# Kernel tuning notes

Measured on AMD Instinct MI355X. Metric: run time of the kernel, lower is better.

## Reference

```python
import jax, jax.numpy as jnp
import numpy as np

N_NODES = 100000


def _sage_conv(x, src, dst, w_self, w_neigh, b):
    # DGL SAGEConv('mean'): fc_self(x) + fc_neigh(mean of in-neighbor feats) + bias
    msgs = x[src]                                        # [E, d] gather
    agg = jax.ops.segment_sum(msgs, dst, num_segments=N_NODES)   # [N, d]
    deg = jax.ops.segment_sum(jnp.ones_like(dst, dtype=x.dtype), dst,
                              num_segments=N_NODES)      # [N]
    mean = agg / jnp.maximum(deg, 1.0)[:, None]          # zero-degree -> 0
    return x @ w_self + mean @ w_neigh + b


def setup_inputs() -> dict:
    key = jax.random.key(0)
    ks = jax.random.split(key, 8)
    E, D_IN, D_HID, D_OUT = 1000000, 64, 64, 32
    features = jax.random.normal(ks[0], (N_NODES, D_IN), dtype=jnp.float32)
    src = jax.random.randint(ks[1], (E,), 0, N_NODES, dtype=jnp.int32)
    dst = jax.random.randint(ks[2], (E,), 0, N_NODES, dtype=jnp.int32)
    s = lambda k, i, o: jax.random.normal(k, (i, o), dtype=jnp.float32) / np.sqrt(i)
    return {
        "features": features, "src": src, "dst": dst,
        "w_self1": s(ks[3], D_IN, D_HID), "w_neigh1": s(ks[4], D_IN, D_HID),
        "b1": jnp.zeros((D_HID,), jnp.float32),
        "w_self2": s(ks[5], D_HID, D_OUT), "w_neigh2": s(ks[6], D_HID, D_OUT),
        "b2": jnp.zeros((D_OUT,), jnp.float32),
    }


def reference(features, src, dst, w_self1, w_neigh1, b1, w_self2, w_neigh2, b2):
    h = _sage_conv(features, src, dst, w_self1, w_neigh1, b1)
    h = jax.nn.relu(h)
    # dropout: identity (inference mode)
    h = _sage_conv(h, src, dst, w_self2, w_neigh2, b2)
    return h
```

## Files before the change

### kernel.cpp

```cpp
#include <hip/hip_runtime.h>


#define SPAN        128
#define SPAN_SHIFT  7
#define PART_BLOCK  1024
#define PART_EPT    4
#define NBMAX       1024
#define LDS_S       72

typedef __attribute__((ext_vector_type(8))) short bf16x8;
typedef __attribute__((ext_vector_type(4))) float f32x4;

__device__ __forceinline__ unsigned bf16_rne(float f) {
    unsigned u = __float_as_uint(f);
    return (u + 0x7FFFu + ((u >> 16) & 1u)) >> 16;
}
__device__ __forceinline__ float bf_lo(unsigned u) { return __uint_as_float(u << 16); }
__device__ __forceinline__ float bf_hi(unsigned u) { return __uint_as_float(u & 0xFFFF0000u); }

__global__ __launch_bounds__(PART_BLOCK) void k_partition(
    const int* __restrict__ src, const int* __restrict__ dst,
    int* __restrict__ cursor, unsigned int* __restrict__ pairs,
    int E, int cap,
    const float* __restrict__ feat, unsigned short* __restrict__ xh, long total8,
    const float* __restrict__ ws1, const float* __restrict__ wn1,
    const float* __restrict__ ws2, const float* __restrict__ wn2,
    unsigned short* __restrict__ wt)
{
    const int tid = threadIdx.x;
    for (long i = (long)blockIdx.x * PART_BLOCK + tid; i < total8;
         i += (long)gridDim.x * PART_BLOCK) {
        const float4 a = ((const float4*)feat)[i * 2];
        const float4 b = ((const float4*)feat)[i * 2 + 1];
        uint4 o;
        o.x = bf16_rne(a.x) | (bf16_rne(a.y) << 16);
        o.y = bf16_rne(a.z) | (bf16_rne(a.w) << 16);
        o.z = bf16_rne(b.x) | (bf16_rne(b.y) << 16);
        o.w = bf16_rne(b.z) | (bf16_rne(b.w) << 16);
        ((uint4*)xh)[i] = o;
    }
    if (blockIdx.x < 12) {
        int j = blockIdx.x * PART_BLOCK + tid;
        int mat = j >> 12, rem = j & 4095;
        int c = rem >> 6, k = rem & 63;
        float v;
        if (mat == 0)      v = ws1[k * 64 + c];
        else if (mat == 1) v = wn1[k * 64 + c];
        else               v = (c < 32) ? wn2[k * 32 + c] : ws2[k * 32 + (c - 32)];
        wt[(mat << 12) + (c << 6) + k] = (unsigned short)bf16_rne(v);
    }

    __shared__ int cnt[NBMAX];
    __shared__ int gbase[NBMAX];
    __shared__ int lcur[NBMAX];
    cnt[tid] = 0; lcur[tid] = 0;
    __syncthreads();

    int sv[PART_EPT], bv[PART_EPT];
    const int e0 = blockIdx.x * (PART_BLOCK * PART_EPT) + tid;
    #pragma unroll
    for (int j = 0; j < PART_EPT; ++j) {
        int e = e0 + j * PART_BLOCK;
        bv[j] = -1;
        if (e < E) {
            int s = src[e], d = dst[e];
            bv[j] = d >> SPAN_SHIFT;
            sv[j] = s | ((d & (SPAN - 1)) << 24);
            atomicAdd(&cnt[bv[j]], 1);
        }
    }
    __syncthreads();
    if (cnt[tid] > 0) gbase[tid] = atomicAdd(&cursor[tid], cnt[tid]);
    __syncthreads();
    #pragma unroll
    for (int j = 0; j < PART_EPT; ++j) {
        if (bv[j] >= 0) {
            int r = gbase[bv[j]] + atomicAdd(&lcur[bv[j]], 1);
            if (r < cap) pairs[(size_t)bv[j] * cap + r] = (unsigned int)sv[j];
        }
    }
}

__global__ __launch_bounds__(256) void k_bucket_csr(
    unsigned int* __restrict__ pairs,
    const int* __restrict__ cursor,
    int* __restrict__ starts, int* __restrict__ degs,
    int N, int cap)
{
    __shared__ int cnt[SPAN];
    __shared__ int pref[SPAN];
    __shared__ int lcur[SPAN];
    extern __shared__ unsigned int sorted[];
    const int tid = threadIdx.x;
    const int b = blockIdx.x;
    if (tid < SPAN) { cnt[tid] = 0; lcur[tid] = 0; }
    __syncthreads();

    int m = cursor[b]; if (m > cap) m = cap;
    const size_t pb = (size_t)b * cap;

    for (int i = tid; i < m; i += 256)
        atomicAdd(&cnt[pairs[pb + i] >> 24], 1);
    __syncthreads();

    if (tid < SPAN) pref[tid] = cnt[tid];
    __syncthreads();
    for (int off = 1; off < SPAN; off <<= 1) {
        int v = 0;
        if (tid < SPAN && tid >= off) v = pref[tid - off];
        __syncthreads();
        if (tid < SPAN) pref[tid] += v;
        __syncthreads();
    }

    for (int i = tid; i < m; i += 256) {
        unsigned int p = pairs[pb + i];
        int r = p >> 24;
        int base = (r == 0) ? 0 : pref[r - 1];
        int pos = base + atomicAdd(&lcur[r], 1);
        sorted[pos] = p & 0xFFFFFFu;
    }
    __syncthreads();
    for (int i = tid; i < m; i += 256) pairs[pb + i] = sorted[i];
    if (tid < SPAN) {
        int node = (b << SPAN_SHIFT) + tid;
        if (node < N) {
            int base = (tid == 0) ? 0 : pref[tid - 1];
            starts[node] = (int)pb + base;
            degs[node]   = cnt[tid];
        }
    }
}

__global__ __launch_bounds__(256) void k_gather_fused(
    const unsigned short* __restrict__ xh,
    const unsigned int* __restrict__ esrc,
    const int* __restrict__ starts, const int* __restrict__ degs,
    const unsigned short* __restrict__ wt,
    const float* __restrict__ b1, const float* __restrict__ b2,
    unsigned short* __restrict__ t2,
    float* __restrict__ outp,
    int n)
{
    __shared__ __align__(16) unsigned short sM[32 * LDS_S];
    __shared__ __align__(16) unsigned short sH[32 * LDS_S];
    const int w = threadIdx.x >> 6, lane = threadIdx.x & 63;
    const int quad = lane >> 4, lm = lane & 15;
    const int half = lane >> 5;
    const int q    = (lane >> 3) & 3;
    const int c    = lane & 7;
    const int gm0  = blockIdx.x * 32;
    const int v0   = gm0 + w * 8;

    int e[4], end[4], dg[4];
    #pragma unroll
    for (int j = 0; j < 4; ++j) {
        int v = v0 + j * 2 + half;
        if (v < n) { int b = starts[v]; dg[j] = degs[v]; e[j] = b + q; end[j] = b + dg[j]; }
        else { dg[j] = 0; e[j] = 0; end[j] = 0; }
    }
    float ga[4][8];
    #pragma unroll
    for (int j = 0; j < 4; ++j)
        #pragma unroll
        for (int k = 0; k < 8; ++k) ga[j][k] = 0.f;

    while ((e[0] < end[0]) | (e[1] < end[1]) | (e[2] < end[2]) | (e[3] < end[3])) {
        uint4 u[4]; float m[4];
        #pragma unroll
        for (int j = 0; j < 4; ++j) {
            bool p = e[j] < end[j];
            m[j] = p ? 1.f : 0.f;
            int idx = p ? e[j] : 0;
            int s = (int)(esrc[idx] & 0xFFFFFFu);
            s = s < n ? s : n - 1;
            u[j] = *(const uint4*)&xh[(size_t)s * 64 + c * 8];
        }
        #pragma unroll
        for (int j = 0; j < 4; ++j) {
            ga[j][0] = fmaf(m[j], bf_lo(u[j].x), ga[j][0]);
            ga[j][1] = fmaf(m[j], bf_hi(u[j].x), ga[j][1]);
            ga[j][2] = fmaf(m[j], bf_lo(u[j].y), ga[j][2]);
            ga[j][3] = fmaf(m[j], bf_hi(u[j].y), ga[j][3]);
            ga[j][4] = fmaf(m[j], bf_lo(u[j].z), ga[j][4]);
            ga[j][5] = fmaf(m[j], bf_hi(u[j].z), ga[j][5]);
            ga[j][6] = fmaf(m[j], bf_lo(u[j].w), ga[j][6]);
            ga[j][7] = fmaf(m[j], bf_hi(u[j].w), ga[j][7]);
            e[j] += 4;
        }
    }
    #pragma unroll
    for (int j = 0; j < 4; ++j) {
        #pragma unroll
        for (int d = 8; d <= 16; d <<= 1) {
            #pragma unroll
            for (int k = 0; k < 8; ++k) ga[j][k] += __shfl_xor(ga[j][k], d);
        }
        int v = v0 + j * 2 + half;
        if ((lane & 24) == 0 && v < n) {
            float f = dg[j] ? 1.f / (float)dg[j] : 0.f;
            uint4 o;
            o.x = bf16_rne(ga[j][0] * f) | (bf16_rne(ga[j][1] * f) << 16);
            o.y = bf16_rne(ga[j][2] * f) | (bf16_rne(ga[j][3] * f) << 16);
            o.z = bf16_rne(ga[j][4] * f) | (bf16_rne(ga[j][5] * f) << 16);
            o.w = bf16_rne(ga[j][6] * f) | (bf16_rne(ga[j][7] * f) << 16);
            *(uint4*)&sM[(w * 8 + j * 2 + half) * LDS_S + c * 8] = o;
        }
    }
    __syncthreads();

    f32x4 acc1[2];
    acc1[0] = (f32x4){0.f, 0.f, 0.f, 0.f};
    acc1[1] = (f32x4){0.f, 0.f, 0.f, 0.f};
    #pragma unroll
    for (int mt = 0; mt < 2; ++mt) {
        const int rowG = gm0 + mt * 16 + lm;
        const int rA = rowG < n ? rowG : n - 1;
        #pragma unroll
        for (int kt = 0; kt < 2; ++kt) {
            bf16x8 a  = *(const bf16x8*)&xh[(size_t)rA * 64 + kt * 32 + quad * 8];
            bf16x8 am = *(const bf16x8*)&sM[(mt * 16 + lm) * LDS_S + kt * 32 + quad * 8];
            bf16x8 bs = *(const bf16x8*)&wt[((w * 16 + lm) << 6) + kt * 32 + quad * 8];
            bf16x8 bn = *(const bf16x8*)&wt[(1 << 12) + ((w * 16 + lm) << 6) + kt * 32 + quad * 8];
            acc1[mt] = __builtin_amdgcn_mfma_f32_16x16x32_bf16(a,  bs, acc1[mt], 0, 0, 0);
            acc1[mt] = __builtin_amdgcn_mfma_f32_16x16x32_bf16(am, bn, acc1[mt], 0, 0, 0);
        }
    }
    {
        float bb = b1[w * 16 + lm];
        #pragma unroll
        for (int mt = 0; mt < 2; ++mt) {
            #pragma unroll
            for (int r = 0; r < 4; ++r) {
                float hv = fmaxf(acc1[mt][r] + bb, 0.f);
                sH[(mt * 16 + quad * 4 + r) * LDS_S + w * 16 + lm] =
                    (unsigned short)bf16_rne(hv);
            }
        }
    }
    __syncthreads();

    f32x4 acc2[2];
    acc2[0] = (f32x4){0.f, 0.f, 0.f, 0.f};
    acc2[1] = (f32x4){0.f, 0.f, 0.f, 0.f};
    #pragma unroll
    for (int mt = 0; mt < 2; ++mt) {
        #pragma unroll
        for (int kt = 0; kt < 2; ++kt) {
            bf16x8 a = *(const bf16x8*)&sH[(mt * 16 + lm) * LDS_S + kt * 32 + quad * 8];
            bf16x8 b = *(const bf16x8*)&wt[(2 << 12) + ((w * 16 + lm) << 6) + kt * 32 + quad * 8];
            acc2[mt] = __builtin_amdgcn_mfma_f32_16x16x32_bf16(a, b, acc2[mt], 0, 0, 0);
        }
    }
    #pragma unroll
    for (int mt = 0; mt < 2; ++mt) {
        if (w < 2) {
            #pragma unroll
            for (int r = 0; r < 4; ++r) {
                int gm = gm0 + mt * 16 + quad * 4 + r;
                if (gm < n)
                    t2[(size_t)gm * 32 + w * 16 + lm] = (unsigned short)bf16_rne(acc2[mt][r]);
            }
        } else {
            float bb = b2[(w - 2) * 16 + lm];
            #pragma unroll
            for (int r = 0; r < 4; ++r) {
                int gm = gm0 + mt * 16 + quad * 4 + r;
                if (gm < n)
                    outp[(size_t)gm * 32 + (w - 2) * 16 + lm] = acc2[mt][r] + bb;
            }
        }
    }
}

__global__ __launch_bounds__(256) void k_gather_b32add(
    const unsigned short* __restrict__ t2,
    const unsigned int* __restrict__ esrc,
    const int* __restrict__ starts, const int* __restrict__ degs,
    float* __restrict__ outp, int n)
{
    const int w = threadIdx.x >> 6, lane = threadIdx.x & 63;
    const int half = lane >> 5;
    const int q    = (lane >> 3) & 3;
    const int c    = lane & 7;
    const int v0 = (blockIdx.x * 4 + w) * 8;
    if (v0 >= n) return;

    int e[4], end[4], dg[4];
    #pragma unroll
    for (int j = 0; j < 4; ++j) {
        int v = v0 + j * 2 + half;
        if (v < n) { int b = starts[v]; dg[j] = degs[v]; e[j] = b + q; end[j] = b + dg[j]; }
        else { dg[j] = 0; e[j] = 0; end[j] = 0; }
    }
    float ga[4][4];
    #pragma unroll
    for (int j = 0; j < 4; ++j)
        #pragma unroll
        for (int k = 0; k < 4; ++k) ga[j][k] = 0.f;

    while ((e[0] < end[0]) | (e[1] < end[1]) | (e[2] < end[2]) | (e[3] < end[3])) {
        uint2 u[4]; float m[4];
        #pragma unroll
        for (int j = 0; j < 4; ++j) {
            bool p = e[j] < end[j];
            m[j] = p ? 1.f : 0.f;
            int idx = p ? e[j] : 0;
            int s = (int)(esrc[idx] & 0xFFFFFFu);
            s = s < n ? s : n - 1;
            u[j] = *(const uint2*)&t2[(size_t)s * 32 + c * 4];
        }
        #pragma unroll
        for (int j = 0; j < 4; ++j) {
            ga[j][0] = fmaf(m[j], bf_lo(u[j].x), ga[j][0]);
            ga[j][1] = fmaf(m[j], bf_hi(u[j].x), ga[j][1]);
            ga[j][2] = fmaf(m[j], bf_lo(u[j].y), ga[j][2]);
            ga[j][3] = fmaf(m[j], bf_hi(u[j].y), ga[j][3]);
            e[j] += 4;
        }
    }
    #pragma unroll
    for (int j = 0; j < 4; ++j) {
        #pragma unroll
        for (int d = 8; d <= 16; d <<= 1) {
            #pragma unroll
            for (int k = 0; k < 4; ++k) ga[j][k] += __shfl_xor(ga[j][k], d);
        }
        int v = v0 + j * 2 + half;
        if ((lane & 24) == 0 && v < n && dg[j] > 0) {
            float f = 1.f / (float)dg[j];
            float4 o = *(const float4*)&outp[(size_t)v * 32 + c * 4];
            o.x += ga[j][0] * f; o.y += ga[j][1] * f;
            o.z += ga[j][2] * f; o.w += ga[j][3] * f;
            *(float4*)&outp[(size_t)v * 32 + c * 4] = o;
        }
    }
}

extern "C" void kernel_launch(void* const* d_in, const int* in_sizes, int n_in,
                              void* d_out, int out_size, void* d_ws, size_t ws_size,
                              hipStream_t stream) {
    const float* feat = (const float*)d_in[0];
    const int*   src  = (const int*)d_in[1];
    const int*   dst  = (const int*)d_in[2];
    const float* ws1  = (const float*)d_in[3];
    const float* wn1  = (const float*)d_in[4];
    const float* b1   = (const float*)d_in[5];
    const float* ws2  = (const float*)d_in[6];
    const float* wn2  = (const float*)d_in[7];
    const float* b2   = (const float*)d_in[8];
    float* out = (float*)d_out;

    const int N = in_sizes[0] / 64;
    const int E = in_sizes[1];
    const int nB = (N + SPAN - 1) >> SPAN_SHIFT;

    int cap = ((E + nB - 1) / nB);
    cap = ((cap + cap / 4) + 63) & ~63;
    {
        size_t fixedBytes = NBMAX * 4 + 3 * 4096 * 2 + (size_t)N * 8
                          + (size_t)N * 64 * 2
                          + (size_t)N * 32 * 2
                          + 16384;
        size_t remain = (ws_size > fixedBytes) ? (ws_size - fixedBytes) : 0;
        size_t capMax = remain / ((size_t)nB * 4);
        if ((size_t)cap > capMax) cap = (int)(capMax & ~(size_t)3);
    }

    char* base = (char*)d_ws;
    int* cursor = (int*)base;
    unsigned short* wt = (unsigned short*)(base + NBMAX * 4);
    unsigned int* pairs = (unsigned int*)(base + NBMAX * 4 + 24576);
    size_t sOff = ((size_t)NBMAX * 4 + 24576 + (size_t)nB * cap * 4 + 4096 + 255) & ~(size_t)255;
    int* starts = (int*)(base + sOff);
    int* degs   = starts + N;
    size_t mOff = (sOff + (size_t)N * 8 + 255) & ~(size_t)255;
    unsigned short* xh = (unsigned short*)(base + mOff);
    unsigned short* t2 = xh + (size_t)N * 64;

    hipMemsetAsync(cursor, 0, NBMAX * 4, stream);

    const long total8 = (long)N * 64 / 8;
    const int pblocks = (E + PART_BLOCK * PART_EPT - 1) / (PART_BLOCK * PART_EPT);
    k_partition<<<pblocks, PART_BLOCK, 0, stream>>>(
        src, dst, cursor, pairs, E, cap,
        feat, xh, total8, ws1, wn1, ws2, wn2, wt);
    k_bucket_csr<<<nB, 256, (size_t)cap * 4, stream>>>(pairs, cursor, starts, degs, N, cap);

    const int fblocks = (N + 31) / 32;

    k_gather_fused<<<fblocks, 256, 0, stream>>>(
        xh, pairs, starts, degs, wt, b1, b2, t2, out, N);
    k_gather_b32add<<<fblocks, 256, 0, stream>>>(t2, pairs, starts, degs, out, N);
}
```

Baseline: 181.5 us.

## Fuse per-bucket CSR sort into both gather kernels using LDS-resident edge lists

Removes the separate bucket-CSR kernel and the global starts/degs arrays. Each gather block instead re-sorts its 128-node bucket's edges into shared memory and reads the neighbour indices from LDS. This saves a kernel launch and a global write/read pass over the pairs, but every bucket is now sorted redundantly by 4 blocks in each of two kernels. Dynamic LDS of up to 8KB per block may also reduce occupancy. Capping cap at 2048 risks dropping edges if a bucket overflows.

Measured after the change: 183.8 us. No clear change (+1.3%).

```diff
diff --git a/kernel.cpp b/kernel.cpp
--- a/kernel.cpp
+++ b/kernel.cpp
@@ -81,28 +81,40 @@
     }
 }
 
-__global__ __launch_bounds__(256) void k_bucket_csr(
-    unsigned int* __restrict__ pairs,
+__global__ __launch_bounds__(256) void k_gather_fused(
+    const unsigned short* __restrict__ xh,
+    const unsigned int* __restrict__ pairs,
     const int* __restrict__ cursor,
-    int* __restrict__ starts, int* __restrict__ degs,
-    int N, int cap)
+    const unsigned short* __restrict__ wt,
+    const float* __restrict__ b1, const float* __restrict__ b2,
+    unsigned short* __restrict__ t2,
+    float* __restrict__ outp,
+    int n, int cap)
 {
+    __shared__ __align__(16) unsigned short sM[32 * LDS_S];
+    __shared__ __align__(16) unsigned short sH[32 * LDS_S];
     __shared__ int cnt[SPAN];
     __shared__ int pref[SPAN];
     __shared__ int lcur[SPAN];
     extern __shared__ unsigned int sorted[];
-    const int tid = threadIdx.x;
-    const int b = blockIdx.x;
+    const int tid  = threadIdx.x;
+    const int w    = tid >> 6, lane = tid & 63;
+    const int quad = lane >> 4, lm = lane & 15;
+    const int half = lane >> 5;
+    const int q    = (lane >> 3) & 3;
+    const int c    = lane & 7;
+    const int gm0  = blockIdx.x * 32;
+    const int B    = gm0 >> SPAN_SHIFT;
+    const int dbase = gm0 & (SPAN - 1);
+
     if (tid < SPAN) { cnt[tid] = 0; lcur[tid] = 0; }
-    __syncthreads();
-
-    int m = cursor[b]; if (m > cap) m = cap;
-    const size_t pb = (size_t)b * cap;
-
+    if (tid == 0) sorted[0] = 0;
+    __syncthreads();
+    int m = cursor[B]; if (m > cap) m = cap;
+    const size_t pb = (size_t)B * cap;
     for (int i = tid; i < m; i += 256)
         atomicAdd(&cnt[pairs[pb + i] >> 24], 1);
     __syncthreads();
-
     if (tid < SPAN) pref[tid] = cnt[tid];
     __syncthreads();
     for (int off = 1; off < SPAN; off <<= 1) {
@@ -112,52 +124,25 @@
         if (tid < SPAN) pref[tid] += v;
         __syncthreads();
     }
-
     for (int i = tid; i < m; i += 256) {
         unsigned int p = pairs[pb + i];
         int r = p >> 24;
-        int base = (r == 0) ? 0 : pref[r - 1];
-        int pos = base + atomicAdd(&lcur[r], 1);
-        sorted[pos] = p & 0xFFFFFFu;
-    }
-    __syncthreads();
-    for (int i = tid; i < m; i += 256) pairs[pb + i] = sorted[i];
-    if (tid < SPAN) {
-        int node = (b << SPAN_SHIFT) + tid;
-        if (node < N) {
-            int base = (tid == 0) ? 0 : pref[tid - 1];
-            starts[node] = (int)pb + base;
-            degs[node]   = cnt[tid];
-        }
-    }
-}
-
-__global__ __launch_bounds__(256) void k_gather_fused(
-    const unsigned short* __restrict__ xh,
-    const unsigned int* __restrict__ esrc,
-    const int* __restrict__ starts, const int* __restrict__ degs,
-    const unsigned short* __restrict__ wt,
-    const float* __restrict__ b1, const float* __restrict__ b2,
-    unsigned short* __restrict__ t2,
-    float* __restrict__ outp,
-    int n)
-{
-    __shared__ __align__(16) unsigned short sM[32 * LDS_S];
-    __shared__ __align__(16) unsigned short sH[32 * LDS_S];
-    const int w = threadIdx.x >> 6, lane = threadIdx.x & 63;
-    const int quad = lane >> 4, lm = lane & 15;
-    const int half = lane >> 5;
-    const int q    = (lane >> 3) & 3;
-    const int c    = lane & 7;
-    const int gm0  = blockIdx.x * 32;
-    const int v0   = gm0 + w * 8;
-
+        int base = r ? pref[r - 1] : 0;
+        sorted[base + atomicAdd(&lcur[r], 1)] = p & 0xFFFFFFu;
+    }
+    __syncthreads();
+
+    const int v0 = gm0 + w * 8;
     int e[4], end[4], dg[4];
     #pragma unroll
     for (int j = 0; j < 4; ++j) {
-        int v = v0 + j * 2 + half;
-        if (v < n) { int b = starts[v]; dg[j] = degs[v]; e[j] = b + q; end[j] = b + dg[j]; }
-        else { dg[j] = 0; e[j] = 0; end[j] = 0; }
+        int no = w * 8 + j * 2 + half;
+        int v  = gm0 + no;
+        int dl = dbase + no;
+        if (v < n) {
+            int bb = dl ? pref[dl - 1] : 0;
+            dg[j] = cnt[dl]; e[j] = bb + q; end[j] = bb + dg[j];
+        } else { dg[j] = 0; e[j] = 0; end[j] = 0; }
     }
     float ga[4][8];
     #pragma unroll
@@ -166,26 +151,26 @@
         for (int k = 0; k < 8; ++k) ga[j][k] = 0.f;
 
     while ((e[0] < end[0]) | (e[1] < end[1]) | (e[2] < end[2]) | (e[3] < end[3])) {
-        uint4 u[4]; float m[4];
+        uint4 u[4]; float mm[4];
         #pragma unroll
         for (int j = 0; j < 4; ++j) {
             bool p = e[j] < end[j];
-            m[j] = p ? 1.f : 0.f;
+            mm[j] = p ? 1.f : 0.f;
             int idx = p ? e[j] : 0;
-            int s = (int)(esrc[idx] & 0xFFFFFFu);
+            int s = (int)sorted[idx];
             s = s < n ? s : n - 1;
             u[j] = *(const uint4*)&xh[(size_t)s * 64 + c * 8];
         }
         #pragma unroll
         for (int j = 0; j < 4; ++j) {
-            ga[j][0] = fmaf(m[j], bf_lo(u[j].x), ga[j][0]);
-            ga[j][1] = fmaf(m[j], bf_hi(u[j].x), ga[j][1]);
-            ga[j][2] = fmaf(m[j], bf_lo(u[j].y), ga[j][2]);
-            ga[j][3] = fmaf(m[j], bf_hi(u[j].y), ga[j][3]);
-            ga[j][4] = fmaf(m[j], bf_lo(u[j].z), ga[j][4]);
-            ga[j][5] = fmaf(m[j], bf_hi(u[j].z), ga[j][5]);
-            ga[j][6] = fmaf(m[j], bf_lo(u[j].w), ga[j][6]);
-            ga[j][7] = fmaf(m[j], bf_hi(u[j].w), ga[j][7]);
+            ga[j][0] = fmaf(mm[j], bf_lo(u[j].x), ga[j][0]);
+            ga[j][1] = fmaf(mm[j], bf_hi(u[j].x), ga[j][1]);
+            ga[j][2] = fmaf(mm[j], bf_lo(u[j].y), ga[j][2]);
+            ga[j][3] = fmaf(mm[j], bf_hi(u[j].y), ga[j][3]);
+            ga[j][4] = fmaf(mm[j], bf_lo(u[j].z), ga[j][4]);
+            ga[j][5] = fmaf(mm[j], bf_hi(u[j].z), ga[j][5]);
+            ga[j][6] = fmaf(mm[j], bf_lo(u[j].w), ga[j][6]);
+            ga[j][7] = fmaf(mm[j], bf_hi(u[j].w), ga[j][7]);
             e[j] += 4;
         }
     }
@@ -275,23 +260,59 @@
 
 __global__ __launch_bounds__(256) void k_gather_b32add(
     const unsigned short* __restrict__ t2,
-    const unsigned int* __restrict__ esrc,
-    const int* __restrict__ starts, const int* __restrict__ degs,
-    float* __restrict__ outp, int n)
+    const unsigned int* __restrict__ pairs,
+    const int* __restrict__ cursor,
+    float* __restrict__ outp, int n, int cap)
 {
-    const int w = threadIdx.x >> 6, lane = threadIdx.x & 63;
+    __shared__ int cnt[SPAN];
+    __shared__ int pref[SPAN];
+    __shared__ int lcur[SPAN];
+    extern __shared__ unsigned int sorted[];
+    const int tid  = threadIdx.x;
+    const int w    = tid >> 6, lane = tid & 63;
     const int half = lane >> 5;
     const int q    = (lane >> 3) & 3;
     const int c    = lane & 7;
-    const int v0 = (blockIdx.x * 4 + w) * 8;
-    if (v0 >= n) return;
-
+    const int gm0  = blockIdx.x * 32;
+    const int B    = gm0 >> SPAN_SHIFT;
+    const int dbase = gm0 & (SPAN - 1);
+
+    if (tid < SPAN) { cnt[tid] = 0; lcur[tid] = 0; }
+    if (tid == 0) sorted[0] = 0;
+    __syncthreads();
+    int m = cursor[B]; if (m > cap) m = cap;
+    const size_t pb = (size_t)B * cap;
+    for (int i = tid; i < m; i += 256)
+        atomicAdd(&cnt[pairs[pb + i] >> 24], 1);
+    __syncthreads();
+    if (tid < SPAN) pref[tid] = cnt[tid];
+    __syncthreads();
+    for (int off = 1; off < SPAN; off <<= 1) {
+        int v = 0;
+        if (tid < SPAN && tid >= off) v = pref[tid - off];
+        __syncthreads();
+        if (tid < SPAN) pref[tid] += v;
+        __syncthreads();
+    }
+    for (int i = tid; i < m; i += 256) {
+        unsigned int p = pairs[pb + i];
+        int r = p >> 24;
+        int base = r ? pref[r - 1] : 0;
+        sorted[base + atomicAdd(&lcur[r], 1)] = p & 0xFFFFFFu;
+    }
+    __syncthreads();
+
+    const int v0 = gm0 + w * 8;
     int e[4], end[4], dg[4];
     #pragma unroll
     for (int j = 0; j < 4; ++j) {
-        int v = v0 + j * 2 + half;
-        if (v < n) { int b = starts[v]; dg[j] = degs[v]; e[j] = b + q; end[j] = b + dg[j]; }
-        else { dg[j] = 0; e[j] = 0; end[j] = 0; }
+        int no = w * 8 + j * 2 + half;
+        int v  = gm0 + no;
+        int dl = dbase + no;
+        if (v < n) {
+            int bb = dl ? pref[dl - 1] : 0;
+            dg[j] = cnt[dl]; e[j] = bb + q; end[j] = bb + dg[j];
+        } else { dg[j] = 0; e[j] = 0; end[j] = 0; }
     }
     float ga[4][4];
     #pragma unroll
@@ -300,22 +321,22 @@
         for (int k = 0; k < 4; ++k) ga[j][k] = 0.f;
 
     while ((e[0] < end[0]) | (e[1] < end[1]) | (e[2] < end[2]) | (e[3] < end[3])) {
-        uint2 u[4]; float m[4];
+        uint2 u[4]; float mm[4];
         #pragma unroll
         for (int j = 0; j < 4; ++j) {
             bool p = e[j] < end[j];
-            m[j] = p ? 1.f : 0.f;
+            mm[j] = p ? 1.f : 0.f;
             int idx = p ? e[j] : 0;
-            int s = (int)(esrc[idx] & 0xFFFFFFu);
+            int s = (int)sorted[idx];
             s = s < n ? s : n - 1;
             u[j] = *(const uint2*)&t2[(size_t)s * 32 + c * 4];
         }
         #pragma unroll
         for (int j = 0; j < 4; ++j) {
-            ga[j][0] = fmaf(m[j], bf_lo(u[j].x), ga[j][0]);
-            ga[j][1] = fmaf(m[j], bf_hi(u[j].x), ga[j][1]);
-            ga[j][2] = fmaf(m[j], bf_lo(u[j].y), ga[j][2]);
-            ga[j][3] = fmaf(m[j], bf_hi(u[j].y), ga[j][3]);
+            ga[j][0] = fmaf(mm[j], bf_lo(u[j].x), ga[j][0]);
+            ga[j][1] = fmaf(mm[j], bf_hi(u[j].x), ga[j][1]);
+            ga[j][2] = fmaf(mm[j], bf_lo(u[j].y), ga[j][2]);
+            ga[j][3] = fmaf(mm[j], bf_hi(u[j].y), ga[j][3]);
             e[j] += 4;
         }
     }
@@ -358,7 +379,7 @@
     int cap = ((E + nB - 1) / nB);
     cap = ((cap + cap / 4) + 63) & ~63;
     {
-        size_t fixedBytes = NBMAX * 4 + 3 * 4096 * 2 + (size_t)N * 8
+        size_t fixedBytes = NBMAX * 4 + 3 * 4096 * 2
                           + (size_t)N * 64 * 2
                           + (size_t)N * 32 * 2
                           + 16384;
@@ -366,15 +387,13 @@
         size_t capMax = remain / ((size_t)nB * 4);
         if ((size_t)cap > capMax) cap = (int)(capMax & ~(size_t)3);
     }
+    if (cap > 2048) cap = 2048;
 
     char* base = (char*)d_ws;
     int* cursor = (int*)base;
     unsigned short* wt = (unsigned short*)(base + NBMAX * 4);
     unsigned int* pairs = (unsigned int*)(base + NBMAX * 4 + 24576);
-    size_t sOff = ((size_t)NBMAX * 4 + 24576 + (size_t)nB * cap * 4 + 4096 + 255) & ~(size_t)255;
-    int* starts = (int*)(base + sOff);
-    int* degs   = starts + N;
-    size_t mOff = (sOff + (size_t)N * 8 + 255) & ~(size_t)255;
+    size_t mOff = ((size_t)NBMAX * 4 + 24576 + (size_t)nB * cap * 4 + 4096 + 255) & ~(size_t)255;
     unsigned short* xh = (unsigned short*)(base + mOff);
     unsigned short* t2 = xh + (size_t)N * 64;
 
@@ -385,11 +404,12 @@
     k_partition<<<pblocks, PART_BLOCK, 0, stream>>>(
         src, dst, cursor, pairs, E, cap,
         feat, xh, total8, ws1, wn1, ws2, wn2, wt);
-    k_bucket_csr<<<nB, 256, (size_t)cap * 4, stream>>>(pairs, cursor, starts, degs, N, cap);
 
     const int fblocks = (N + 31) / 32;
-
-    k_gather_fused<<<fblocks, 256, 0, stream>>>(
-        xh, pairs, starts, degs, wt, b1, b2, t2, out, N);
-    k_gather_b32add<<<fblocks, 256, 0, stream>>>(t2, pairs, starts, degs, out, N);
+    const size_t dynLds = (size_t)cap * 4;
+
+    k_gather_fused<<<fblocks, 256, dynLds, stream>>>(
+        xh, pairs, cursor, wt, b1, b2, t2, out, N, cap);
+    k_gather_b32add<<<fblocks, 256, dynLds, stream>>>(
+        t2, pairs, cursor, out, N, cap);
 }
```
